# Kernel optimization log

Hardware: AMD Instinct MI355X
Metric: run time of the kernel (lower is better)

## Reference

```python
import jax, jax.numpy as jnp
import numpy as np

N_NODES = 50000
N_FEATURES = 128
HIDDEN = 64
N_EDGES = 1600000


def gcn_conv(x, src, dst, edge_w, W, b, num_nodes):
    """torch_geometric GCNConv with edge weights: add self-loops (weight 1),
    symmetric deg^-1/2 normalization, aggregate into dst, then bias."""
    loop = jnp.arange(num_nodes)
    src_f = jnp.concatenate([src, loop])
    dst_f = jnp.concatenate([dst, loop])
    w_f = jnp.concatenate([edge_w, jnp.ones((num_nodes,), dtype=edge_w.dtype)])
    deg = jax.ops.segment_sum(w_f, dst_f, num_segments=num_nodes)
    dinv = jnp.where(deg > 0, jax.lax.rsqrt(deg), 0.0)
    norm = dinv[src_f] * w_f * dinv[dst_f]            # [E+N]
    h = x @ W                                          # [N, out]
    msg = h[src_f] * norm[:, None]                     # [E+N, out]
    out = jax.ops.segment_sum(msg, dst_f, num_segments=num_nodes)
    return out + b


def setup_inputs() -> dict:
    key = jax.random.key(0)
    ks = jax.random.split(key, 12)
    features = jax.random.normal(ks[0], (N_NODES, N_FEATURES), dtype=jnp.float32)
    edge_index = jax.random.randint(ks[1], (2, N_EDGES), 0, N_NODES, dtype=jnp.int64)
    edge_attr = jax.random.uniform(ks[2], (N_EDGES,), dtype=jnp.float32)
    s = 0.05
    W1 = jax.random.normal(ks[3], (N_FEATURES, HIDDEN), dtype=jnp.float32) * s
    b1 = jnp.zeros((HIDDEN,), dtype=jnp.float32)
    W2 = jax.random.normal(ks[4], (HIDDEN, HIDDEN // 2), dtype=jnp.float32) * s
    b2 = jnp.zeros((HIDDEN // 2,), dtype=jnp.float32)
    Wd = jax.random.normal(ks[5], (N_FEATURES, 2), dtype=jnp.float32) * s
    bd = jnp.zeros((2,), dtype=jnp.float32)
    w_fc = jax.random.normal(ks[6], (N_NODES * 2,), dtype=jnp.float32) * s
    b_fc = jnp.zeros((), dtype=jnp.float32)
    return {"features": features, "edge_index": edge_index, "edge_attr": edge_attr,
            "W1": W1, "b1": b1, "W2": W2, "b2": b2, "Wd": Wd, "bd": bd,
            "w_fc": w_fc, "b_fc": b_fc}


def reference(features, edge_index, edge_attr, W1, b1, W2, b2, Wd, bd, w_fc, b_fc):
    N = features.shape[0]
    src, dst = edge_index[0], edge_index[1]
    # --- generator encoder (GAE.encode): GCN -> relu -> GCN -> tanh ---
    h = gcn_conv(features, src, dst, edge_attr, W1, b1, N)
    h = jax.nn.relu(h)                                  # dropout inactive (eval)
    z = jnp.tanh(gcn_conv(h, src, dst, edge_attr, W2, b2, N))  # [N, HIDDEN//2]
    # --- residual path: tile z to n_features width and add input features ---
    rep = features.shape[1] // z.shape[1]
    x = jnp.tile(z, (1, rep)) + features                # [N, n_features]
    # (edge_probabilities = z@z.T + rebuilt adjacency is computed by the
    #  generator but discarded by GraphCounteRGAN.forward -> dead code)
    # --- discriminator: GCN -> relu -> flatten -> fc -> sigmoid ---
    d = jax.nn.relu(gcn_conv(x, src, dst, edge_attr, Wd, bd, N))  # [N, 2]
    logit = jnp.dot(d.reshape(-1), w_fc) + b_fc
    return jax.nn.sigmoid(logit)
```

## Files before the change

kernel.cpp:

```cpp
#include <hip/hip_runtime.h>
#include <math.h>

#define BLK 256
#define CHUNK 4096
#define BSH 7
#define BNODES 128
#define MAXNB 512

__device__ __forceinline__ unsigned short f2bf(float f) {
    unsigned u = __float_as_uint(f);
    u += 0x7FFFu + ((u >> 16) & 1u);
    return (unsigned short)(u >> 16);
}
__device__ __forceinline__ float bf2f(unsigned short b) {
    return __uint_as_float(((unsigned)b) << 16);
}

__global__ void detect_kernel(const int* __restrict__ idx, int E,
                              int* __restrict__ flag, float* __restrict__ acc) {
    int t = threadIdx.x;
    long long j = (long long)t * (E / 64);
    int hi = idx[2 * j + 1];
    unsigned long long b = __ballot(hi != 0);
    if (t == 0) { *flag = (b == 0ULL) ? 1 : 0; *acc = 0.f; }
}

__global__ __launch_bounds__(256) void bucket_hist_kernel(const int* __restrict__ idx,
                                                          const int* __restrict__ flag,
                                                          int* __restrict__ blockCnt,
                                                          int E, int NB) {
    __shared__ int hist[MAXNB];
    int t = threadIdx.x;
    for (int i = t; i < NB; i += 256) hist[i] = 0;
    __syncthreads();
    bool i64 = (*flag) != 0;
    int e0 = blockIdx.x * CHUNK;
    int e1 = min(e0 + CHUNK, E);
    for (int e = e0 + t; e < e1; e += 256) {
        int d = i64 ? idx[2 * (E + e)] : idx[E + e];
        atomicAdd(&hist[d >> BSH], 1);
    }
    __syncthreads();
    for (int i = t; i < NB; i += 256) blockCnt[blockIdx.x * NB + i] = hist[i];
}

__global__ __launch_bounds__(256) void col_scan_kernel(const int* __restrict__ blockCnt,
                                                       int* __restrict__ blockBase,
                                                       int* __restrict__ bucketTotal,
                                                       int NBLK, int NB) {
    __shared__ int s[256];
    __shared__ int carry;
    int bkt = blockIdx.x;
    int t = threadIdx.x;
    if (t == 0) carry = 0;
    __syncthreads();
    for (int base = 0; base < NBLK; base += 256) {
        int i = base + t;
        int v = (i < NBLK) ? blockCnt[i * NB + bkt] : 0;
        s[t] = v;
        __syncthreads();
        for (int off = 1; off < 256; off <<= 1) {
            int x = (t >= off) ? s[t - off] : 0;
            __syncthreads();
            s[t] += x;
            __syncthreads();
        }
        if (i < NBLK) blockBase[i * NB + bkt] = carry + s[t] - v;
        __syncthreads();
        if (t == 0) carry += s[255];
        __syncthreads();
    }
    if (t == 0) bucketTotal[bkt] = carry;
}

__global__ __launch_bounds__(512) void bucket_scan_kernel(const int* __restrict__ bucketTotal,
                                                          int* __restrict__ bucketBase, int NB) {
    __shared__ int s[512];
    int t = threadIdx.x;
    int v = (t < NB) ? bucketTotal[t] : 0;
    s[t] = v;
    __syncthreads();
    for (int off = 1; off < 512; off <<= 1) {
        int x = (t >= off) ? s[t - off] : 0;
        __syncthreads();
        s[t] += x;
        __syncthreads();
    }
    if (t < NB) bucketBase[t] = s[t] - v;
}

__global__ __launch_bounds__(256) void bucket_scatter_kernel(const int* __restrict__ idx,
                                                             const float* __restrict__ ew,
                                                             const int* __restrict__ flag,
                                                             const int* __restrict__ bucketBase,
                                                             const int* __restrict__ blockBase,
                                                             int2* __restrict__ temp,
                                                             int E, int NB) {
    __shared__ int base[MAXNB];
    __shared__ int fill[MAXNB];
    int t = threadIdx.x;
    for (int i = t; i < NB; i += 256) {
        base[i] = bucketBase[i] + blockBase[blockIdx.x * NB + i];
        fill[i] = 0;
    }
    __syncthreads();
    bool i64 = (*flag) != 0;
    int e0 = blockIdx.x * CHUNK;
    int e1 = min(e0 + CHUNK, E);
    for (int e = e0 + t; e < e1; e += 256) {
        int s_, d;
        if (i64) { s_ = idx[2 * e]; d = idx[2 * (E + e)]; }
        else     { s_ = idx[e];     d = idx[E + e]; }
        float w = ew[e];
        int b = d >> BSH;
        int pos = base[b] + atomicAdd(&fill[b], 1);
        temp[pos] = make_int2(s_ | ((d & (BNODES - 1)) << 16), __float_as_int(w));
    }
}

__global__ __launch_bounds__(512) void csr_build_kernel(const int2* __restrict__ temp,
                                                        const int* __restrict__ bucketBase,
                                                        unsigned* __restrict__ csrw,
                                                        int* __restrict__ row,
                                                        float* __restrict__ dinv,
                                                        int N, int NB, int E) {
    __shared__ int cnt[BNODES];
    __shared__ float dw[BNODES];
    __shared__ int offs[BNODES];
    int bkt = blockIdx.x;
    int t = threadIdx.x;
    int node0 = bkt << BSH;
    int nn = min(BNODES, N - node0);
    if (t < BNODES) { cnt[t] = 0; dw[t] = 0.f; }
    __syncthreads();
    int p0 = bucketBase[bkt];
    int p1 = (bkt + 1 < NB) ? bucketBase[bkt + 1] : E;
    for (int p = p0 + t; p < p1; p += 512) {
        int2 v = temp[p];
        int dl = (v.x >> 16) & (BNODES - 1);
        atomicAdd(&cnt[dl], 1);
        atomicAdd(&dw[dl], __int_as_float(v.y));
    }
    __syncthreads();
    int v = 0;
    if (t < BNODES) { v = cnt[t]; offs[t] = v; }
    __syncthreads();
    for (int off = 1; off < BNODES; off <<= 1) {
        int x = 0;
        if (t < BNODES && t >= off) x = offs[t - off];
        __syncthreads();
        if (t < BNODES) offs[t] += x;
        __syncthreads();
    }
    if (t < BNODES) {
        int excl = offs[t] - v;
        if (t < nn) {
            row[node0 + t] = p0 + excl;
            dinv[node0 + t] = rsqrtf(1.f + dw[t]);
        }
        offs[t] = excl;
    }
    if (bkt == NB - 1 && t == 0) row[N] = E;
    __syncthreads();
    if (t < BNODES) cnt[t] = 0;
    __syncthreads();
    for (int p = p0 + t; p < p1; p += 512) {
        int2 v2 = temp[p];
        int dl = (v2.x >> 16) & (BNODES - 1);
        int pos = p0 + offs[dl] + atomicAdd(&cnt[dl], 1);
        unsigned wb = (unsigned)v2.y;
        wb += 0x7FFFu + ((wb >> 16) & 1u);
        csrw[pos] = ((unsigned)v2.x & 0xFFFFu) | (wb & 0xFFFF0000u);
    }
}

__global__ void norm_kernel(unsigned* __restrict__ csrw, const float* __restrict__ dinv, int E) {
    int e = blockIdx.x * BLK + threadIdx.x;
    if (e >= E) return;
    unsigned pe = csrw[e];
    float w = __uint_as_float(pe & 0xFFFF0000u) * dinv[pe & 0xFFFFu];
    unsigned wb = __float_as_uint(w);
    wb += 0x7FFFu + ((wb >> 16) & 1u);
    csrw[e] = (pe & 0xFFFFu) | (wb & 0xFFFF0000u);
}

__global__ __launch_bounds__(256) void gather64_kernel(const int* __restrict__ row,
                                                       const unsigned* __restrict__ csrw,
                                                       const unsigned short* __restrict__ h,
                                                       const float* __restrict__ dinv,
                                                       const float* __restrict__ bias,
                                                       float* __restrict__ out, int N) {
    int wid = (blockIdx.x * 256 + threadIdx.x) >> 6;
    int o = threadIdx.x & 63;
    if (wid >= N) return;
    float di = dinv[wid];
    int p0 = row[wid], p1 = row[wid + 1];
    const unsigned short* hb = h + o;
    float es0 = 0.f, es1 = 0.f;
    for (int p = p0; p < p1; p += 64) {
        int q = p + o;
        unsigned pe = (q < p1) ? csrw[q] : 0u;
        int m = min(64, p1 - p);
        int mp = (m + 7) & ~7;
        for (int j = 0; j < mp; j += 8) {
            unsigned e0 = (unsigned)__shfl((int)pe, j + 0, 64);
            unsigned e1 = (unsigned)__shfl((int)pe, j + 1, 64);
            unsigned e2 = (unsigned)__shfl((int)pe, j + 2, 64);
            unsigned e3 = (unsigned)__shfl((int)pe, j + 3, 64);
            unsigned e4 = (unsigned)__shfl((int)pe, j + 4, 64);
            unsigned e5 = (unsigned)__shfl((int)pe, j + 5, 64);
            unsigned e6 = (unsigned)__shfl((int)pe, j + 6, 64);
            unsigned e7 = (unsigned)__shfl((int)pe, j + 7, 64);
            float h0 = bf2f(hb[(e0 & 0xFFFFu) * 64]);
            float h1 = bf2f(hb[(e1 & 0xFFFFu) * 64]);
            float h2 = bf2f(hb[(e2 & 0xFFFFu) * 64]);
            float h3 = bf2f(hb[(e3 & 0xFFFFu) * 64]);
            float h4 = bf2f(hb[(e4 & 0xFFFFu) * 64]);
            float h5 = bf2f(hb[(e5 & 0xFFFFu) * 64]);
            float h6 = bf2f(hb[(e6 & 0xFFFFu) * 64]);
            float h7 = bf2f(hb[(e7 & 0xFFFFu) * 64]);
            es0 = fmaf(__uint_as_float(e0 & 0xFFFF0000u), h0, es0);
            es1 = fmaf(__uint_as_float(e1 & 0xFFFF0000u), h1, es1);
            es0 = fmaf(__uint_as_float(e2 & 0xFFFF0000u), h2, es0);
            es1 = fmaf(__uint_as_float(e3 & 0xFFFF0000u), h3, es1);
            es0 = fmaf(__uint_as_float(e4 & 0xFFFF0000u), h4, es0);
            es1 = fmaf(__uint_as_float(e5 & 0xFFFF0000u), h5, es1);
            es0 = fmaf(__uint_as_float(e6 & 0xFFFF0000u), h6, es0);
            es1 = fmaf(__uint_as_float(e7 & 0xFFFF0000u), h7, es1);
        }
    }
    out[wid * 64 + o] = bias[o] + di * (di * bf2f(h[(size_t)wid * 64 + o]) + es0 + es1);
}

__global__ __launch_bounds__(256) void gather32_kernel(const int* __restrict__ row,
                                                       const unsigned* __restrict__ csrw,
                                                       const unsigned short* __restrict__ h,
                                                       const float* __restrict__ dinv,
                                                       const float* __restrict__ bias,
                                                       float* __restrict__ out, int N) {
    int wid = (blockIdx.x * 256 + threadIdx.x) >> 6;
    int lane = threadIdx.x & 63;
    int o = lane & 31;
    int g = lane >> 5;
    if (wid >= N) return;
    float di = dinv[wid];
    int p0 = row[wid], p1 = row[wid + 1];
    const unsigned short* hb = h + o;
    float es0 = 0.f, es1 = 0.f;
    for (int p = p0; p < p1; p += 64) {
        int q = p + lane;
        unsigned pe = (q < p1) ? csrw[q] : 0u;
        int m = min(64, p1 - p);
        int mp = (m + 7) & ~7;
        for (int j = g; j < mp; j += 8) {
            unsigned e0 = (unsigned)__shfl((int)pe, j + 0, 64);
            unsigned e1 = (unsigned)__shfl((int)pe, j + 2, 64);
            unsigned e2 = (unsigned)__shfl((int)pe, j + 4, 64);
            unsigned e3 = (unsigned)__shfl((int)pe, j + 6, 64);
            float h0 = bf2f(hb[(e0 & 0xFFFFu) * 32]);
            float h1 = bf2f(hb[(e1 & 0xFFFFu) * 32]);
            float h2 = bf2f(hb[(e2 & 0xFFFFu) * 32]);
            float h3 = bf2f(hb[(e3 & 0xFFFFu) * 32]);
            es0 = fmaf(__uint_as_float(e0 & 0xFFFF0000u), h0, es0);
            es1 = fmaf(__uint_as_float(e1 & 0xFFFF0000u), h1, es1);
            es0 = fmaf(__uint_as_float(e2 & 0xFFFF0000u), h2, es0);
            es1 = fmaf(__uint_as_float(e3 & 0xFFFF0000u), h3, es1);
        }
    }
    float es = es0 + es1;
    es += __shfl_down(es, 32, 64);
    if (g == 0) out[wid * 32 + o] = bias[o] + di * (di * bf2f(h[wid * 32 + o]) + es);
}

__global__ __launch_bounds__(256) void gather2_kernel(const int* __restrict__ row,
                                                      const unsigned* __restrict__ csrw,
                                                      const unsigned short* __restrict__ h,
                                                      const float* __restrict__ dinv,
                                                      const float* __restrict__ bias,
                                                      float* __restrict__ out, int N) {
    const unsigned* hp = (const unsigned*)h;
    int wid = (blockIdx.x * 256 + threadIdx.x) >> 6;
    int lane = threadIdx.x & 63;
    if (wid >= N) return;
    float di = dinv[wid];
    int p0 = row[wid], p1 = row[wid + 1];
    float a0 = 0.f, a1 = 0.f, b0 = 0.f, b1 = 0.f;
    int p = p0 + lane;
    for (; p + 64 < p1; p += 128) {
        unsigned pe0 = csrw[p];
        unsigned pe1 = csrw[p + 64];
        unsigned hw0 = hp[pe0 & 0xFFFFu];
        unsigned hw1 = hp[pe1 & 0xFFFFu];
        float w0 = __uint_as_float(pe0 & 0xFFFF0000u);
        float w1 = __uint_as_float(pe1 & 0xFFFF0000u);
        a0 = fmaf(w0, __uint_as_float(hw0 << 16), a0);
        a1 = fmaf(w0, __uint_as_float(hw0 & 0xFFFF0000u), a1);
        b0 = fmaf(w1, __uint_as_float(hw1 << 16), b0);
        b1 = fmaf(w1, __uint_as_float(hw1 & 0xFFFF0000u), b1);
    }
    if (p < p1) {
        unsigned pe0 = csrw[p];
        unsigned hw0 = hp[pe0 & 0xFFFFu];
        float w0 = __uint_as_float(pe0 & 0xFFFF0000u);
        a0 = fmaf(w0, __uint_as_float(hw0 << 16), a0);
        a1 = fmaf(w0, __uint_as_float(hw0 & 0xFFFF0000u), a1);
    }
    a0 += b0; a1 += b1;
#pragma unroll
    for (int off = 32; off > 0; off >>= 1) {
        a0 += __shfl_down(a0, off, 64);
        a1 += __shfl_down(a1, off, 64);
    }
    if (lane == 0) {
        unsigned hw = hp[wid];
        out[wid * 2 + 0] = bias[0] + di * (di * __uint_as_float(hw << 16) + a0);
        out[wid * 2 + 1] = bias[1] + di * (di * __uint_as_float(hw & 0xFFFF0000u) + a1);
    }
}

__global__ __launch_bounds__(256) void mm1_kernel(const float* __restrict__ X,
                                                  const float* __restrict__ W,
                                                  unsigned short* __restrict__ Y, int N) {
    __shared__ float Xs[32 * 132];
    __shared__ uint2 Wsb[128 * 16];
    const float4* Wg = (const float4*)W;
    for (int i = threadIdx.x; i < 128 * 16; i += 256) {
        float4 wv = Wg[i];
        unsigned lo = ((unsigned)f2bf(wv.x)) | (((unsigned)f2bf(wv.y)) << 16);
        unsigned hi = ((unsigned)f2bf(wv.z)) | (((unsigned)f2bf(wv.w)) << 16);
        Wsb[i] = make_uint2(lo, hi);
    }
    int row0 = blockIdx.x * 32;
    for (int i = threadIdx.x; i < 32 * 128; i += 256) {
        int r = i >> 7, k = i & 127;
        int rr = row0 + r;
        Xs[r * 132 + k] = (rr < N) ? X[(size_t)rr * 128 + k] : 0.f;
    }
    __syncthreads();
    int r0 = (threadIdx.x >> 4) * 2;
    int c4 = threadIdx.x & 15;
    float4 a0 = {0.f, 0.f, 0.f, 0.f};
    float4 a1 = {0.f, 0.f, 0.f, 0.f};
#pragma unroll 4
    for (int k = 0; k < 128; ++k) {
        float x0 = Xs[r0 * 132 + k];
        float x1 = Xs[(r0 + 1) * 132 + k];
        uint2 wp = Wsb[k * 16 + c4];
        float w0 = __uint_as_float(wp.x << 16);
        float w1 = __uint_as_float(wp.x & 0xFFFF0000u);
        float w2 = __uint_as_float(wp.y << 16);
        float w3 = __uint_as_float(wp.y & 0xFFFF0000u);
        a0.x = fmaf(x0, w0, a0.x); a0.y = fmaf(x0, w1, a0.y);
        a0.z = fmaf(x0, w2, a0.z); a0.w = fmaf(x0, w3, a0.w);
        a1.x = fmaf(x1, w0, a1.x); a1.y = fmaf(x1, w1, a1.y);
        a1.z = fmaf(x1, w2, a1.z); a1.w = fmaf(x1, w3, a1.w);
    }
    int row = row0 + r0;
    if (row < N) {
        ushort4 o;
        o.x = f2bf(a0.x); o.y = f2bf(a0.y); o.z = f2bf(a0.z); o.w = f2bf(a0.w);
        ((ushort4*)Y)[(size_t)row * 16 + c4] = o;
    }
    if (row + 1 < N) {
        ushort4 o;
        o.x = f2bf(a1.x); o.y = f2bf(a1.y); o.z = f2bf(a1.z); o.w = f2bf(a1.w);
        ((ushort4*)Y)[(size_t)(row + 1) * 16 + c4] = o;
    }
}

__global__ __launch_bounds__(256) void mm2_kernel(const float* __restrict__ H,
                                                  const float* __restrict__ W,
                                                  unsigned short* __restrict__ Y, int N) {
    __shared__ float Xs[32 * 68];
    __shared__ float4 Ws[64 * 8];
    const float4* Wg = (const float4*)W;
    for (int i = threadIdx.x; i < 64 * 8; i += 256) Ws[i] = Wg[i];
    int row0 = blockIdx.x * 32;
    for (int i = threadIdx.x; i < 32 * 64; i += 256) {
        int r = i >> 6, k = i & 63;
        int row = row0 + r;
        Xs[r * 68 + k] = (row < N) ? fmaxf(H[row * 64 + k], 0.f) : 0.f;
    }
    __syncthreads();
    int r = threadIdx.x >> 3;
    int c4 = threadIdx.x & 7;
    int row = row0 + r;
    float4 acc = {0.f, 0.f, 0.f, 0.f};
#pragma unroll 4
    for (int k = 0; k < 64; ++k) {
        float xv = Xs[r * 68 + k];
        float4 wv = Ws[k * 8 + c4];
        acc.x = fmaf(xv, wv.x, acc.x);
        acc.y = fmaf(xv, wv.y, acc.y);
        acc.z = fmaf(xv, wv.z, acc.z);
        acc.w = fmaf(xv, wv.w, acc.w);
    }
    if (row < N) {
        ushort4 o;
        o.x = f2bf(acc.x); o.y = f2bf(acc.y); o.z = f2bf(acc.z); o.w = f2bf(acc.w);
        ((ushort4*)Y)[row * 8 + c4] = o;
    }
}

__global__ __launch_bounds__(256) void disc_mm_kernel(const float* __restrict__ Z,
                                                      const float* __restrict__ F,
                                                      const float* __restrict__ Wd,
                                                      unsigned short* __restrict__ Y, int N) {
    __shared__ float Ws[256];
    if (threadIdx.x < 256) Ws[threadIdx.x] = Wd[threadIdx.x];
    __syncthreads();
    int n = blockIdx.x * 256 + threadIdx.x;
    if (n >= N) return;
    float zt[32];
#pragma unroll
    for (int j = 0; j < 32; ++j) zt[j] = tanhf(Z[n * 32 + j]);
    float a0 = 0.f, a1 = 0.f;
    const float* fr = F + (size_t)n * 128;
#pragma unroll 4
    for (int c = 0; c < 128; ++c) {
        float xv = zt[c & 31] + fr[c];
        a0 = fmaf(xv, Ws[c * 2 + 0], a0);
        a1 = fmaf(xv, Ws[c * 2 + 1], a1);
    }
    ushort2 o;
    o.x = f2bf(a0); o.y = f2bf(a1);
    ((ushort2*)Y)[n] = o;
}

__global__ void init_deg_kernel(float* __restrict__ deg, int N) {
    int n = blockIdx.x * BLK + threadIdx.x;
    if (n < N) deg[n] = 1.0f;
}

__global__ void edge_deg_kernel(const int* __restrict__ idx, const float* __restrict__ ew,
                                const int* __restrict__ flag, float* __restrict__ deg, int E) {
    int e = blockIdx.x * BLK + threadIdx.x;
    if (e >= E) return;
    int d = (*flag) ? idx[2 * (E + e)] : idx[E + e];
    atomicAdd(&deg[d], ew[e]);
}

__global__ void dinv_kernel(float* __restrict__ deg, int N) {
    int n = blockIdx.x * BLK + threadIdx.x;
    if (n < N) deg[n] = rsqrtf(deg[n]);
}

template <int WD>
__global__ void init_agg_kernel(const unsigned short* __restrict__ h, const float* __restrict__ dinv,
                                const float* __restrict__ bias, float* __restrict__ agg, int N) {
    int i = blockIdx.x * BLK + threadIdx.x;
    if (i >= N * WD) return;
    int n = i / WD, o = i % WD;
    float di = dinv[n];
    agg[i] = bias[o] + di * di * bf2f(h[i]);
}

template <int WD>
__global__ void edge_agg_kernel(const int* __restrict__ idx, const float* __restrict__ ew,
                                const int* __restrict__ flag, const float* __restrict__ dinv,
                                const unsigned short* __restrict__ h, float* __restrict__ agg, int E) {
    int gid = blockIdx.x * BLK + threadIdx.x;
    if (gid >= E * WD) return;
    int e = gid / WD;
    int o = gid % WD;
    int s, d;
    if (*flag) { s = idx[2 * e]; d = idx[2 * (E + e)]; }
    else       { s = idx[e];     d = idx[E + e]; }
    float nrm = dinv[s] * ew[e] * dinv[d];
    atomicAdd(&agg[d * WD + o], nrm * bf2f(h[s * WD + o]));
}

__global__ void reduce_kernel(const float* __restrict__ dmat, const float* __restrict__ wfc,
                              float* __restrict__ acc, int M) {
    int i = blockIdx.x * BLK + threadIdx.x;
    float v = 0.f;
    if (i < M) v = fmaxf(dmat[i], 0.f) * wfc[i];
#pragma unroll
    for (int off = 32; off > 0; off >>= 1) v += __shfl_down(v, off, 64);
    if ((threadIdx.x & 63) == 0) atomicAdd(acc, v);
}

__global__ void final_kernel(const float* __restrict__ acc, const float* __restrict__ bfc,
                             float* __restrict__ out) {
    float x = *acc + *bfc;
    out[0] = 1.f / (1.f + expf(-x));
}

extern "C" void kernel_launch(void* const* d_in, const int* in_sizes, int n_in,
                              void* d_out, int out_size, void* d_ws, size_t ws_size,
                              hipStream_t stream) {
    const float* feat = (const float*)d_in[0];
    const int*   eidx = (const int*)d_in[1];
    const float* ew   = (const float*)d_in[2];
    const float* W1   = (const float*)d_in[3];
    const float* b1   = (const float*)d_in[4];
    const float* W2   = (const float*)d_in[5];
    const float* b2   = (const float*)d_in[6];
    const float* Wd   = (const float*)d_in[7];
    const float* bd   = (const float*)d_in[8];
    const float* wfc  = (const float*)d_in[9];
    const float* bfc  = (const float*)d_in[10];

    const int N = in_sizes[0] / 128;
    const int E = in_sizes[2];

    const int NB   = (N + BNODES - 1) >> BSH;
    const int NBLK = (E + CHUNK - 1) / CHUNK;

    float* ws = (float*)d_ws;
    size_t u = 0;
    float* dinv = ws + u; u += N;
    if (u & 1) u++;
    size_t M1 = ((size_t)N * 32 > (size_t)E * 2) ? (size_t)N * 32 : (size_t)E * 2;
    unsigned short* h = (unsigned short*)(ws + u); int2* temp = (int2*)h; u += M1;
    if (u & 1) u++;
    float* agg = ws + u; u += (size_t)N * 64;
    float* acc = ws + u; u += 1;
    int* flag = (int*)(ws + u); u += 1;
    int* row  = (int*)(ws + u); u += (size_t)N + 1;
    int* bucketTotal = (int*)(ws + u); u += NB;
    int* bucketBase  = (int*)(ws + u); u += NB + 1;
    int* blockCnt    = (int*)(ws + u); u += (size_t)NBLK * NB;
    int* blockBase   = (int*)(ws + u); u += (size_t)NBLK * NB;
    unsigned* csrw   = (unsigned*)(ws + u); u += (size_t)E;
    size_t need = u * 4;

    float* out = (float*)d_out;

    const int gN = (N + BLK - 1) / BLK;
    const int gE = (E + BLK - 1) / BLK;
    const int gW = (N + 3) / 4;

    if (ws_size >= need && N <= 65536 && NB <= MAXNB) {
        hipLaunchKernelGGL(detect_kernel, dim3(1), dim3(64), 0, stream, eidx, E, flag, acc);
        hipLaunchKernelGGL(bucket_hist_kernel, dim3(NBLK), dim3(256), 0, stream,
                           eidx, flag, blockCnt, E, NB);
        hipLaunchKernelGGL(col_scan_kernel, dim3(NB), dim3(256), 0, stream,
                           blockCnt, blockBase, bucketTotal, NBLK, NB);
        hipLaunchKernelGGL(bucket_scan_kernel, dim3(1), dim3(512), 0, stream,
                           bucketTotal, bucketBase, NB);
        hipLaunchKernelGGL(bucket_scatter_kernel, dim3(NBLK), dim3(256), 0, stream,
                           eidx, ew, flag, bucketBase, blockBase, temp, E, NB);
        hipLaunchKernelGGL(csr_build_kernel, dim3(NB), dim3(512), 0, stream,
                           temp, bucketBase, csrw, row, dinv, N, NB, E);
        hipLaunchKernelGGL(norm_kernel, dim3(gE), dim3(BLK), 0, stream, csrw, dinv, E);

        hipLaunchKernelGGL(mm1_kernel, dim3((N + 31) / 32), dim3(256), 0, stream, feat, W1, h, N);
        hipLaunchKernelGGL(gather64_kernel, dim3(gW), dim3(256), 0, stream,
                           row, csrw, h, dinv, b1, agg, N);
        hipLaunchKernelGGL(mm2_kernel, dim3((N + 31) / 32), dim3(256), 0, stream, agg, W2, h, N);
        hipLaunchKernelGGL(gather32_kernel, dim3(gW), dim3(256), 0, stream,
                           row, csrw, h, dinv, b2, agg, N);
        hipLaunchKernelGGL(disc_mm_kernel, dim3((N + 255) / 256), dim3(256), 0, stream,
                           agg, feat, Wd, h, N);
        hipLaunchKernelGGL(gather2_kernel, dim3(gW), dim3(256), 0, stream,
                           row, csrw, h, dinv, bd, agg, N);
    } else {
        hipLaunchKernelGGL(detect_kernel, dim3(1), dim3(64), 0, stream, eidx, E, flag, acc);
        hipLaunchKernelGGL(init_deg_kernel, dim3(gN), dim3(BLK), 0, stream, dinv, N);
        hipLaunchKernelGGL(edge_deg_kernel, dim3(gE), dim3(BLK), 0, stream, eidx, ew, flag, dinv, E);
        hipLaunchKernelGGL(dinv_kernel, dim3(gN), dim3(BLK), 0, stream, dinv, N);

        hipLaunchKernelGGL(mm1_kernel, dim3((N + 31) / 32), dim3(256), 0, stream, feat, W1, h, N);
        hipLaunchKernelGGL((init_agg_kernel<64>), dim3((N * 64 + BLK - 1) / BLK), dim3(BLK), 0, stream,
                           h, dinv, b1, agg, N);
        hipLaunchKernelGGL((edge_agg_kernel<64>), dim3((E / BLK) * 64 + 64), dim3(BLK), 0, stream,
                           eidx, ew, flag, dinv, h, agg, E);
        hipLaunchKernelGGL(mm2_kernel, dim3((N + 31) / 32), dim3(256), 0, stream, agg, W2, h, N);
        hipLaunchKernelGGL((init_agg_kernel<32>), dim3((N * 32 + BLK - 1) / BLK), dim3(BLK), 0, stream,
                           h, dinv, b2, agg, N);
        hipLaunchKernelGGL((edge_agg_kernel<32>), dim3((E / BLK) * 32 + 32), dim3(BLK), 0, stream,
                           eidx, ew, flag, dinv, h, agg, E);
        hipLaunchKernelGGL(disc_mm_kernel, dim3((N + 255) / 256), dim3(256), 0, stream,
                           agg, feat, Wd, h, N);
        hipLaunchKernelGGL((init_agg_kernel<2>), dim3((N * 2 + BLK - 1) / BLK), dim3(BLK), 0, stream,
                           h, dinv, bd, agg, N);
        hipLaunchKernelGGL((edge_agg_kernel<2>), dim3((E * 2 + BLK - 1) / BLK), dim3(BLK), 0, stream,
                           eidx, ew, flag, dinv, h, agg, E);
    }

    hipLaunchKernelGGL(reduce_kernel, dim3((N * 2 + BLK - 1) / BLK), dim3(BLK), 0, stream,
                       agg, wfc, acc, N * 2);
    hipLaunchKernelGGL(final_kernel, dim3(1), dim3(1), 0, stream, acc, bfc, out);
}
```

Baseline: 310.6 us.

## Inline index-width detection, fuse final reduce, widen gather unroll, larger buckets

Removes the separate detect kernel by having each histogram and scatter block compute the int64/int32 check itself. Fuses the final reduce and sigmoid into one kernel that uses a last-block-done counter. Deepens the gather64 and gather32 inner loops to 16 edges per step with four accumulators, so more independent loads are in flight. Doubles the CSR bucket size to 256 nodes, which cuts the number of buckets and the cost of the scans. In exchange it adds redundant detection loads in every block and relies on a threadfence and atomic pattern for the fused final step.

```diff
diff --git a/kernel.cpp b/kernel.cpp
--- a/kernel.cpp
+++ b/kernel.cpp
@@ -3,9 +3,9 @@
 
 #define BLK 256
 #define CHUNK 4096
-#define BSH 7
-#define BNODES 128
-#define MAXNB 512
+#define BSH 8
+#define BNODES 256
+#define MAXNB 256
 
 __device__ __forceinline__ unsigned short f2bf(float f) {
     unsigned u = __float_as_uint(f);
@@ -17,23 +17,30 @@
 }
 
 __global__ void detect_kernel(const int* __restrict__ idx, int E,
-                              int* __restrict__ flag, float* __restrict__ acc) {
+                              int* __restrict__ flag, float* __restrict__ acc,
+                              int* __restrict__ done) {
     int t = threadIdx.x;
     long long j = (long long)t * (E / 64);
     int hi = idx[2 * j + 1];
     unsigned long long b = __ballot(hi != 0);
-    if (t == 0) { *flag = (b == 0ULL) ? 1 : 0; *acc = 0.f; }
+    if (t == 0) { *flag = (b == 0ULL) ? 1 : 0; *acc = 0.f; *done = 0; }
 }
 
 __global__ __launch_bounds__(256) void bucket_hist_kernel(const int* __restrict__ idx,
-                                                          const int* __restrict__ flag,
                                                           int* __restrict__ blockCnt,
                                                           int E, int NB) {
     __shared__ int hist[MAXNB];
+    __shared__ int i64s;
     int t = threadIdx.x;
     for (int i = t; i < NB; i += 256) hist[i] = 0;
-    __syncthreads();
-    bool i64 = (*flag) != 0;
+    if (t < 64) {
+        long long j = (long long)t * (E / 64);
+        int hi = idx[2 * j + 1];
+        unsigned long long b = __ballot(hi != 0);
+        if (t == 0) i64s = (b == 0ULL) ? 1 : 0;
+    }
+    __syncthreads();
+    bool i64 = i64s != 0;
     int e0 = blockIdx.x * CHUNK;
     int e1 = min(e0 + CHUNK, E);
     for (int e = e0 + t; e < e1; e += 256) {
@@ -73,14 +80,17 @@
     if (t == 0) bucketTotal[bkt] = carry;
 }
 
-__global__ __launch_bounds__(512) void bucket_scan_kernel(const int* __restrict__ bucketTotal,
-                                                          int* __restrict__ bucketBase, int NB) {
-    __shared__ int s[512];
+__global__ __launch_bounds__(256) void bucket_scan_kernel(const int* __restrict__ bucketTotal,
+                                                          int* __restrict__ bucketBase, int NB,
+                                                          float* __restrict__ acc,
+                                                          int* __restrict__ done) {
+    __shared__ int s[256];
     int t = threadIdx.x;
+    if (t == 0) { *acc = 0.f; *done = 0; }
     int v = (t < NB) ? bucketTotal[t] : 0;
     s[t] = v;
     __syncthreads();
-    for (int off = 1; off < 512; off <<= 1) {
+    for (int off = 1; off < 256; off <<= 1) {
         int x = (t >= off) ? s[t - off] : 0;
         __syncthreads();
         s[t] += x;
@@ -91,20 +101,26 @@
 
 __global__ __launch_bounds__(256) void bucket_scatter_kernel(const int* __restrict__ idx,
                                                              const float* __restrict__ ew,
-                                                             const int* __restrict__ flag,
                                                              const int* __restrict__ bucketBase,
                                                              const int* __restrict__ blockBase,
                                                              int2* __restrict__ temp,
                                                              int E, int NB) {
     __shared__ int base[MAXNB];
     __shared__ int fill[MAXNB];
+    __shared__ int i64s;
     int t = threadIdx.x;
     for (int i = t; i < NB; i += 256) {
         base[i] = bucketBase[i] + blockBase[blockIdx.x * NB + i];
         fill[i] = 0;
     }
-    __syncthreads();
-    bool i64 = (*flag) != 0;
+    if (t < 64) {
+        long long j = (long long)t * (E / 64);
+        int hi = idx[2 * j + 1];
+        unsigned long long b = __ballot(hi != 0);
+        if (t == 0) i64s = (b == 0ULL) ? 1 : 0;
+    }
+    __syncthreads();
+    bool i64 = i64s != 0;
     int e0 = blockIdx.x * CHUNK;
     int e1 = min(e0 + CHUNK, E);
     for (int e = e0 + t; e < e1; e += 256) {
@@ -196,40 +212,26 @@
     float di = dinv[wid];
     int p0 = row[wid], p1 = row[wid + 1];
     const unsigned short* hb = h + o;
-    float es0 = 0.f, es1 = 0.f;
+    float es[4] = {0.f, 0.f, 0.f, 0.f};
     for (int p = p0; p < p1; p += 64) {
         int q = p + o;
         unsigned pe = (q < p1) ? csrw[q] : 0u;
         int m = min(64, p1 - p);
-        int mp = (m + 7) & ~7;
-        for (int j = 0; j < mp; j += 8) {
-            unsigned e0 = (unsigned)__shfl((int)pe, j + 0, 64);
-            unsigned e1 = (unsigned)__shfl((int)pe, j + 1, 64);
-            unsigned e2 = (unsigned)__shfl((int)pe, j + 2, 64);
-            unsigned e3 = (unsigned)__shfl((int)pe, j + 3, 64);
-            unsigned e4 = (unsigned)__shfl((int)pe, j + 4, 64);
-            unsigned e5 = (unsigned)__shfl((int)pe, j + 5, 64);
-            unsigned e6 = (unsigned)__shfl((int)pe, j + 6, 64);
-            unsigned e7 = (unsigned)__shfl((int)pe, j + 7, 64);
-            float h0 = bf2f(hb[(e0 & 0xFFFFu) * 64]);
-            float h1 = bf2f(hb[(e1 & 0xFFFFu) * 64]);
-            float h2 = bf2f(hb[(e2 & 0xFFFFu) * 64]);
-            float h3 = bf2f(hb[(e3 & 0xFFFFu) * 64]);
-            float h4 = bf2f(hb[(e4 & 0xFFFFu) * 64]);
-            float h5 = bf2f(hb[(e5 & 0xFFFFu) * 64]);
-            float h6 = bf2f(hb[(e6 & 0xFFFFu) * 64]);
-            float h7 = bf2f(hb[(e7 & 0xFFFFu) * 64]);
-            es0 = fmaf(__uint_as_float(e0 & 0xFFFF0000u), h0, es0);
-            es1 = fmaf(__uint_as_float(e1 & 0xFFFF0000u), h1, es1);
-            es0 = fmaf(__uint_as_float(e2 & 0xFFFF0000u), h2, es0);
-            es1 = fmaf(__uint_as_float(e3 & 0xFFFF0000u), h3, es1);
-            es0 = fmaf(__uint_as_float(e4 & 0xFFFF0000u), h4, es0);
-            es1 = fmaf(__uint_as_float(e5 & 0xFFFF0000u), h5, es1);
-            es0 = fmaf(__uint_as_float(e6 & 0xFFFF0000u), h6, es0);
-            es1 = fmaf(__uint_as_float(e7 & 0xFFFF0000u), h7, es1);
+        int mp = (m + 15) & ~15;
+        for (int j = 0; j < mp; j += 16) {
+            unsigned ee[16];
+            float hh[16];
+#pragma unroll
+            for (int u = 0; u < 16; ++u) ee[u] = (unsigned)__shfl((int)pe, j + u, 64);
+#pragma unroll
+            for (int u = 0; u < 16; ++u) hh[u] = bf2f(hb[(ee[u] & 0xFFFFu) * 64]);
+#pragma unroll
+            for (int u = 0; u < 16; ++u)
+                es[u & 3] = fmaf(__uint_as_float(ee[u] & 0xFFFF0000u), hh[u], es[u & 3]);
         }
     }
-    out[wid * 64 + o] = bias[o] + di * (di * bf2f(h[(size_t)wid * 64 + o]) + es0 + es1);
+    float e01 = es[0] + es[1], e23 = es[2] + es[3];
+    out[wid * 64 + o] = bias[o] + di * (di * bf2f(h[(size_t)wid * 64 + o]) + e01 + e23);
 }
 
 __global__ __launch_bounds__(256) void gather32_kernel(const int* __restrict__ row,
@@ -246,30 +248,27 @@
     float di = dinv[wid];
     int p0 = row[wid], p1 = row[wid + 1];
     const unsigned short* hb = h + o;
-    float es0 = 0.f, es1 = 0.f;
+    float es[4] = {0.f, 0.f, 0.f, 0.f};
     for (int p = p0; p < p1; p += 64) {
         int q = p + lane;
         unsigned pe = (q < p1) ? csrw[q] : 0u;
         int m = min(64, p1 - p);
-        int mp = (m + 7) & ~7;
-        for (int j = g; j < mp; j += 8) {
-            unsigned e0 = (unsigned)__shfl((int)pe, j + 0, 64);
-            unsigned e1 = (unsigned)__shfl((int)pe, j + 2, 64);
-            unsigned e2 = (unsigned)__shfl((int)pe, j + 4, 64);
-            unsigned e3 = (unsigned)__shfl((int)pe, j + 6, 64);
-            float h0 = bf2f(hb[(e0 & 0xFFFFu) * 32]);
-            float h1 = bf2f(hb[(e1 & 0xFFFFu) * 32]);
-            float h2 = bf2f(hb[(e2 & 0xFFFFu) * 32]);
-            float h3 = bf2f(hb[(e3 & 0xFFFFu) * 32]);
-            es0 = fmaf(__uint_as_float(e0 & 0xFFFF0000u), h0, es0);
-            es1 = fmaf(__uint_as_float(e1 & 0xFFFF0000u), h1, es1);
-            es0 = fmaf(__uint_as_float(e2 & 0xFFFF0000u), h2, es0);
-            es1 = fmaf(__uint_as_float(e3 & 0xFFFF0000u), h3, es1);
+        int mp = (m + 15) & ~15;
+        for (int j = g; j < mp; j += 16) {
+            unsigned ee[8];
+            float hh[8];
+#pragma unroll
+            for (int u = 0; u < 8; ++u) ee[u] = (unsigned)__shfl((int)pe, j + 2 * u, 64);
+#pragma unroll
+            for (int u = 0; u < 8; ++u) hh[u] = bf2f(hb[(ee[u] & 0xFFFFu) * 32]);
+#pragma unroll
+            for (int u = 0; u < 8; ++u)
+                es[u & 3] = fmaf(__uint_as_float(ee[u] & 0xFFFF0000u), hh[u], es[u & 3]);
         }
     }
-    float es = es0 + es1;
-    es += __shfl_down(es, 32, 64);
-    if (g == 0) out[wid * 32 + o] = bias[o] + di * (di * bf2f(h[wid * 32 + o]) + es);
+    float es_t = (es[0] + es[1]) + (es[2] + es[3]);
+    es_t += __shfl_down(es_t, 32, 64);
+    if (g == 0) out[wid * 32 + o] = bias[o] + di * (di * bf2f(h[wid * 32 + o]) + es_t);
 }
 
 __global__ __launch_bounds__(256) void gather2_kernel(const int* __restrict__ row,
@@ -470,20 +469,25 @@
     atomicAdd(&agg[d * WD + o], nrm * bf2f(h[s * WD + o]));
 }
 
-__global__ void reduce_kernel(const float* __restrict__ dmat, const float* __restrict__ wfc,
-                              float* __restrict__ acc, int M) {
+__global__ void reduce_final_kernel(const float* __restrict__ dmat, const float* __restrict__ wfc,
+                                    float* __restrict__ acc, int* __restrict__ done,
+                                    const float* __restrict__ bfc, float* __restrict__ out,
+                                    int M, int nblk) {
     int i = blockIdx.x * BLK + threadIdx.x;
     float v = 0.f;
     if (i < M) v = fmaxf(dmat[i], 0.f) * wfc[i];
 #pragma unroll
     for (int off = 32; off > 0; off >>= 1) v += __shfl_down(v, off, 64);
     if ((threadIdx.x & 63) == 0) atomicAdd(acc, v);
-}
-
-__global__ void final_kernel(const float* __restrict__ acc, const float* __restrict__ bfc,
-                             float* __restrict__ out) {
-    float x = *acc + *bfc;
-    out[0] = 1.f / (1.f + expf(-x));
+    __syncthreads();
+    if (threadIdx.x == 0) {
+        __threadfence();
+        int old = atomicAdd(done, 1);
+        if (old == nblk - 1) {
+            float x = atomicAdd(acc, 0.f) + *bfc;
+            out[0] = 1.f / (1.f + expf(-x));
+        }
+    }
 }
 
 extern "C" void kernel_launch(void* const* d_in, const int* in_sizes, int n_in,
@@ -517,6 +521,7 @@
     float* agg = ws + u; u += (size_t)N * 64;
     float* acc = ws + u; u += 1;
     int* flag = (int*)(ws + u); u += 1;
+    int* done = (int*)(ws + u); u += 1;
     int* row  = (int*)(ws + u); u += (size_t)N + 1;
     int* bucketTotal = (int*)(ws + u); u += NB;
     int* bucketBase  = (int*)(ws + u); u += NB + 1;
@@ -530,17 +535,17 @@
     const int gN = (N + BLK - 1) / BLK;
     const int gE = (E + BLK - 1) / BLK;
     const int gW = (N + 3) / 4;
+    const int gR = (N * 2 + BLK - 1) / BLK;
 
     if (ws_size >= need && N <= 65536 && NB <= MAXNB) {
-        hipLaunchKernelGGL(detect_kernel, dim3(1), dim3(64), 0, stream, eidx, E, flag, acc);
         hipLaunchKernelGGL(bucket_hist_kernel, dim3(NBLK), dim3(256), 0, stream,
-                           eidx, flag, blockCnt, E, NB);
+                           eidx, blockCnt, E, NB);
         hipLaunchKernelGGL(col_scan_kernel, dim3(NB), dim3(256), 0, stream,
                            blockCnt, blockBase, bucketTotal, NBLK, NB);
-        hipLaunchKernelGGL(bucket_scan_kernel, dim3(1), dim3(512), 0, stream,
-                           bucketTotal, bucketBase, NB);
+        hipLaunchKernelGGL(bucket_scan_kernel, dim3(1), dim3(256), 0, stream,
+                           bucketTotal, bucketBase, NB, acc, done);
         hipLaunchKernelGGL(bucket_scatter_kernel, dim3(NBLK), dim3(256), 0, stream,
-                           eidx, ew, flag, bucketBase, blockBase, temp, E, NB);
+                           eidx, ew, bucketBase, blockBase, temp, E, NB);
         hipLaunchKernelGGL(csr_build_kernel, dim3(NB), dim3(512), 0, stream,
                            temp, bucketBase, csrw, row, dinv, N, NB, E);
         hipLaunchKernelGGL(norm_kernel, dim3(gE), dim3(BLK), 0, stream, csrw, dinv, E);
@@ -556,7 +561,7 @@
         hipLaunchKernelGGL(gather2_kernel, dim3(gW), dim3(256), 0, stream,
                            row, csrw, h, dinv, bd, agg, N);
     } else {
-        hipLaunchKernelGGL(detect_kernel, dim3(1), dim3(64), 0, stream, eidx, E, flag, acc);
+        hipLaunchKernelGGL(detect_kernel, dim3(1), dim3(64), 0, stream, eidx, E, flag, acc, done);
         hipLaunchKernelGGL(init_deg_kernel, dim3(gN), dim3(BLK), 0, stream, dinv, N);
         hipLaunchKernelGGL(edge_deg_kernel, dim3(gE), dim3(BLK), 0, stream, eidx, ew, flag, dinv, E);
         hipLaunchKernelGGL(dinv_kernel, dim3(gN), dim3(BLK), 0, stream, dinv, N);
@@ -579,7 +584,6 @@
                            eidx, ew, flag, dinv, h, agg, E);
     }
 
-    hipLaunchKernelGGL(reduce_kernel, dim3((N * 2 + BLK - 1) / BLK), dim3(BLK), 0, stream,
-                       agg, wfc, acc, N * 2);
-    hipLaunchKernelGGL(final_kernel, dim3(1), dim3(1), 0, stream, acc, bfc, out);
-}
+    hipLaunchKernelGGL(reduce_final_kernel, dim3(gR), dim3(BLK), 0, stream,
+                       agg, wfc, acc, done, bfc, out, N * 2, gR);
+}
```

Result: faster. 298.5 us (-3.9%).
